# Optimization experiments

Hardware: AMD Instinct MI355X
Metric: run time of the kernel (lower is better)

Reference implementation:

```python
import jax, jax.numpy as jnp
import numpy as np

N_NODES = 100000
N_EDGES = 1600000
D_FEAT = 64


def setup_inputs() -> dict:
    key = jax.random.key(0)
    k1, k2, k3, k4 = jax.random.split(key, 4)
    row = jnp.sort(jax.random.randint(k1, (N_EDGES,), 0, N_NODES, dtype=jnp.int32))
    col = jax.random.randint(k2, (N_EDGES,), 0, N_NODES, dtype=jnp.int32)
    values = jax.random.uniform(k3, (N_EDGES,), dtype=jnp.float32)
    x = jax.random.normal(k4, (N_NODES, D_FEAT), dtype=jnp.float32)
    return {"row": row, "col": col, "values": values, "x": x}


def reference(row, col, values, x):
    # spmm_scatter: out[row[e]] += values[e] * x[col[e]]  (gather-multiply-scatter)
    msgs = x[col] * values[:, None]                      # [E, d]
    out = jax.ops.segment_sum(msgs, row, num_segments=x.shape[0])  # [N, d]
    return out
```

## Files before the change

kernel.cpp:

```cpp
#include <hip/hip_runtime.h>
#include <hip/hip_fp16.h>


constexpr int D  = 64;
constexpr int DV = 16;
constexpr int DH = 16;

struct __align__(8) h4 { __half2 a, b; };

__global__ __launch_bounds__(256) void prep_kernel(
    const int* __restrict__ row,
    const float4* __restrict__ x4,
    h4* __restrict__ xh,
    int* __restrict__ row_ptr,
    int nEdges, int n4, int nNodes)
{
    const int i = blockIdx.x * blockDim.x + threadIdx.x;
    if (i < n4) {
        const float4 v = x4[i];
        h4 h;
        h.a = __float22half2_rn(make_float2(v.x, v.y));
        h.b = __float22half2_rn(make_float2(v.z, v.w));
        xh[i] = h;
    }
    if (i < nEdges) {
        const int r    = row[i];
        const int prev = (i == 0) ? -1 : row[i - 1];
        for (int n = prev + 1; n <= r; ++n) row_ptr[n] = i;
        if (i == nEdges - 1)
            for (int n = r + 1; n <= nNodes; ++n) row_ptr[n] = nEdges;
    }
}

__global__ __launch_bounds__(256) void spmm_h(
    const int* __restrict__ row_ptr,
    const int* __restrict__ col,
    const float* __restrict__ val,
    const h4* __restrict__ xh,
    float4* __restrict__ out4,
    int nNodes)
{
    const int wid = (blockIdx.x * blockDim.x + threadIdx.x) >> 6;
    if (wid >= nNodes) return;
    const int lane  = threadIdx.x & 63;
    const int group = lane >> 4;
    const int sub   = lane & 15;

    const int start = row_ptr[wid];
    const int end   = row_ptr[wid + 1];

    float4 acc = {0.f, 0.f, 0.f, 0.f};
    for (int e = start + group; e < end; e += 16) {
        const int e1 = e + 4, e2 = e + 8, e3 = e + 12;
        const int   c0 = col[e];
        const float v0 = val[e];
        int c1 = c0, c2 = c0, c3 = c0;
        float v1 = 0.f, v2 = 0.f, v3 = 0.f;
        if (e1 < end) { c1 = col[e1]; v1 = val[e1]; }
        if (e2 < end) { c2 = col[e2]; v2 = val[e2]; }
        if (e3 < end) { c3 = col[e3]; v3 = val[e3]; }
        const h4 p0 = xh[(size_t)c0 * DH + sub];
        const h4 p1 = xh[(size_t)c1 * DH + sub];
        const h4 p2 = xh[(size_t)c2 * DH + sub];
        const h4 p3 = xh[(size_t)c3 * DH + sub];
        float2 f;
        f = __half22float2(p0.a); acc.x = fmaf(v0, f.x, acc.x); acc.y = fmaf(v0, f.y, acc.y);
        f = __half22float2(p0.b); acc.z = fmaf(v0, f.x, acc.z); acc.w = fmaf(v0, f.y, acc.w);
        f = __half22float2(p1.a); acc.x = fmaf(v1, f.x, acc.x); acc.y = fmaf(v1, f.y, acc.y);
        f = __half22float2(p1.b); acc.z = fmaf(v1, f.x, acc.z); acc.w = fmaf(v1, f.y, acc.w);
        f = __half22float2(p2.a); acc.x = fmaf(v2, f.x, acc.x); acc.y = fmaf(v2, f.y, acc.y);
        f = __half22float2(p2.b); acc.z = fmaf(v2, f.x, acc.z); acc.w = fmaf(v2, f.y, acc.w);
        f = __half22float2(p3.a); acc.x = fmaf(v3, f.x, acc.x); acc.y = fmaf(v3, f.y, acc.y);
        f = __half22float2(p3.b); acc.z = fmaf(v3, f.x, acc.z); acc.w = fmaf(v3, f.y, acc.w);
    }

    #pragma unroll
    for (int off = 16; off <= 32; off <<= 1) {
        acc.x += __shfl_xor(acc.x, off, 64);
        acc.y += __shfl_xor(acc.y, off, 64);
        acc.z += __shfl_xor(acc.z, off, 64);
        acc.w += __shfl_xor(acc.w, off, 64);
    }
    if (group == 0) out4[(size_t)wid * DV + sub] = acc;
}

__global__ __launch_bounds__(256) void spmm_psearch(
    const int* __restrict__ row,
    const int* __restrict__ col,
    const float* __restrict__ val,
    const float4* __restrict__ x4,
    float4* __restrict__ out4,
    int nEdges, int nNodes)
{
    const int wid = (blockIdx.x * blockDim.x + threadIdx.x) >> 6;
    if (wid >= nNodes) return;
    const int lane  = threadIdx.x & 63;
    const int group = lane >> 4;
    const int sub   = lane & 15;

    int lo = 0, hi = nEdges;
    const int t0 = wid;
    while (hi > lo) {
        const int span = hi - lo + 1;
        if (span <= 64) {
            const int idx = lo + lane;
            const bool lt = (idx <= hi) && (idx < nEdges) && (row[idx] < t0);
            lo += __popcll(__ballot(lt));
            break;
        }
        const int step = (span + 63) >> 6;
        const int idx  = lo + lane * step;
        const bool lt  = (idx <= hi) && (idx < nEdges) && (row[idx] < t0);
        const int  c   = __popcll(__ballot(lt));
        if (c == 0) { hi = lo; break; }
        const int new_lo = lo + (c - 1) * step + 1;
        if (c < 64) hi = lo + c * step;
        lo = new_lo;
    }
    const int start = lo;
    const int t1 = wid + 1;
    int end = start;
    for (;;) {
        const int idx = end + lane;
        const bool lt = (idx < nEdges) && (row[idx] < t1);
        const int  c  = __popcll(__ballot(lt));
        end += c;
        if (c < 64) break;
    }

    float4 acc = {0.f, 0.f, 0.f, 0.f};
    for (int e = start + group; e < end; e += 8) {
        const int e1 = e + 4;
        const int   c0 = col[e];
        const float v0 = val[e];
        int c1 = c0; float v1 = 0.f;
        if (e1 < end) { c1 = col[e1]; v1 = val[e1]; }
        const float4 x0 = x4[(size_t)c0 * DV + sub];
        const float4 x1 = x4[(size_t)c1 * DV + sub];
        acc.x = fmaf(v0, x0.x, acc.x); acc.y = fmaf(v0, x0.y, acc.y);
        acc.z = fmaf(v0, x0.z, acc.z); acc.w = fmaf(v0, x0.w, acc.w);
        acc.x = fmaf(v1, x1.x, acc.x); acc.y = fmaf(v1, x1.y, acc.y);
        acc.z = fmaf(v1, x1.z, acc.z); acc.w = fmaf(v1, x1.w, acc.w);
    }
    #pragma unroll
    for (int off = 16; off <= 32; off <<= 1) {
        acc.x += __shfl_xor(acc.x, off, 64);
        acc.y += __shfl_xor(acc.y, off, 64);
        acc.z += __shfl_xor(acc.z, off, 64);
        acc.w += __shfl_xor(acc.w, off, 64);
    }
    if (group == 0) out4[(size_t)wid * DV + sub] = acc;
}

extern "C" void kernel_launch(void* const* d_in, const int* in_sizes, int n_in,
                              void* d_out, int out_size, void* d_ws, size_t ws_size,
                              hipStream_t stream)
{
    const int*    row  = (const int*)   d_in[0];
    const int*    col  = (const int*)   d_in[1];
    const float*  val  = (const float*) d_in[2];
    const float4* x4   = (const float4*)d_in[3];
    float4*       out4 = (float4*)d_out;

    const int nEdges = in_sizes[0];
    const int nNodes = out_size / D;
    const int n4     = nNodes * DV;

    const dim3 block(256);
    const dim3 gridMain(((size_t)nNodes * 64 + 255) / 256);

    const size_t rp_bytes = (size_t)(nNodes + 1) * sizeof(int);
    const size_t xh_off   = (rp_bytes + 255) & ~(size_t)255;
    const size_t need     = xh_off + (size_t)nNodes * D * sizeof(__half);

    if (ws_size >= need) {
        int* row_ptr = (int*)d_ws;
        h4*  xh      = (h4*)((char*)d_ws + xh_off);
        const int prep_n = (nEdges > n4) ? nEdges : n4;
        prep_kernel<<<dim3((prep_n + 255) / 256), block, 0, stream>>>(
            row, x4, xh, row_ptr, nEdges, n4, nNodes);
        spmm_h<<<gridMain, block, 0, stream>>>(
            row_ptr, (const int*)d_in[1], val, xh, out4, nNodes);
    } else {
        spmm_psearch<<<gridMain, block, 0, stream>>>(
            row, (const int*)d_in[1], val, x4, out4, nEdges, nNodes);
    }
}
```

Before: 135.4 us.

## Use 16-byte half8 gathers and cooperative edge-index loads with shuffle broadcast

Widens each lane's fp16 gather of x from 8 to 16 bytes, so 8 lanes cover a 64-feature row and 8 edge groups run in parallel. The first 64 edges of a row have their col/val loaded once per wave, one per lane, and are then broadcast with shuffles, replacing redundant per-group index loads. The prep kernel now converts two float4s per thread. The cost is more shuffles, a three-step reduction over 8 accumulators, and a tail loop for rows with more than 64 edges.

```diff
diff --git a/kernel.cpp b/kernel.cpp
--- a/kernel.cpp
+++ b/kernel.cpp
@@ -2,25 +2,28 @@
 #include <hip/hip_fp16.h>
 
 
-constexpr int D  = 64;
-constexpr int DV = 16;
-constexpr int DH = 16;
-
-struct __align__(8) h4 { __half2 a, b; };
+constexpr int D   = 64;
+constexpr int DV  = 16;
+constexpr int DH8 = 8;
+
+struct __align__(16) h8 { __half2 a, b, c, d; };
 
 __global__ __launch_bounds__(256) void prep_kernel(
     const int* __restrict__ row,
     const float4* __restrict__ x4,
-    h4* __restrict__ xh,
+    h8* __restrict__ xh,
     int* __restrict__ row_ptr,
-    int nEdges, int n4, int nNodes)
+    int nEdges, int n8, int nNodes)
 {
     const int i = blockIdx.x * blockDim.x + threadIdx.x;
-    if (i < n4) {
-        const float4 v = x4[i];
-        h4 h;
-        h.a = __float22half2_rn(make_float2(v.x, v.y));
-        h.b = __float22half2_rn(make_float2(v.z, v.w));
+    if (i < n8) {
+        const float4 lo = x4[2 * i];
+        const float4 hi = x4[2 * i + 1];
+        h8 h;
+        h.a = __float22half2_rn(make_float2(lo.x, lo.y));
+        h.b = __float22half2_rn(make_float2(lo.z, lo.w));
+        h.c = __float22half2_rn(make_float2(hi.x, hi.y));
+        h.d = __float22half2_rn(make_float2(hi.z, hi.w));
         xh[i] = h;
     }
     if (i < nEdges) {
@@ -32,56 +35,77 @@
     }
 }
 
-__global__ __launch_bounds__(256) void spmm_h(
+__device__ __forceinline__ void fma_h8(const h8& p, float v, float4& a0, float4& a1)
+{
+    float2 f;
+    f = __half22float2(p.a); a0.x = fmaf(v, f.x, a0.x); a0.y = fmaf(v, f.y, a0.y);
+    f = __half22float2(p.b); a0.z = fmaf(v, f.x, a0.z); a0.w = fmaf(v, f.y, a0.w);
+    f = __half22float2(p.c); a1.x = fmaf(v, f.x, a1.x); a1.y = fmaf(v, f.y, a1.y);
+    f = __half22float2(p.d); a1.z = fmaf(v, f.x, a1.z); a1.w = fmaf(v, f.y, a1.w);
+}
+
+__global__ __launch_bounds__(256) void spmm_h8(
     const int* __restrict__ row_ptr,
     const int* __restrict__ col,
     const float* __restrict__ val,
-    const h4* __restrict__ xh,
+    const h8* __restrict__ xh,
     float4* __restrict__ out4,
     int nNodes)
 {
     const int wid = (blockIdx.x * blockDim.x + threadIdx.x) >> 6;
     if (wid >= nNodes) return;
-    const int lane  = threadIdx.x & 63;
-    const int group = lane >> 4;
-    const int sub   = lane & 15;
-
-    const int start = row_ptr[wid];
-    const int end   = row_ptr[wid + 1];
-
-    float4 acc = {0.f, 0.f, 0.f, 0.f};
-    for (int e = start + group; e < end; e += 16) {
-        const int e1 = e + 4, e2 = e + 8, e3 = e + 12;
-        const int   c0 = col[e];
-        const float v0 = val[e];
-        int c1 = c0, c2 = c0, c3 = c0;
-        float v1 = 0.f, v2 = 0.f, v3 = 0.f;
+    const int lane = threadIdx.x & 63;
+    const int g    = lane >> 3;
+    const int sub  = lane & 7;
+
+    const int uw    = __builtin_amdgcn_readfirstlane(wid);
+    const int start = row_ptr[uw];
+    const int end   = row_ptr[uw + 1];
+    const int deg   = end - start;
+
+    const int  eL  = start + lane;
+    const bool okL = eL < end;
+    const int   cv = okL ? col[eL] : 0;
+    const float vv = okL ? val[eL] : 0.f;
+
+    float4 a0 = {0.f, 0.f, 0.f, 0.f};
+    float4 a1 = {0.f, 0.f, 0.f, 0.f};
+
+    const int it64 = min((deg + 15) >> 4, 4);
+    for (int it = 0; it < it64; ++it) {
+        const int s0 = it * 16 + 2 * g;
+        const int   c0 = __shfl(cv, s0, 64);
+        const float v0 = __shfl(vv, s0, 64);
+        const int   c1 = __shfl(cv, s0 + 1, 64);
+        const float v1 = __shfl(vv, s0 + 1, 64);
+        const h8 p0 = xh[(size_t)c0 * DH8 + sub];
+        const h8 p1 = xh[(size_t)c1 * DH8 + sub];
+        fma_h8(p0, v0, a0, a1);
+        fma_h8(p1, v1, a0, a1);
+    }
+
+    for (int ebase = start + 64; ebase < end; ebase += 16) {
+        const int e0 = ebase + 2 * g, e1 = e0 + 1;
+        int c0 = 0, c1 = 0; float v0 = 0.f, v1 = 0.f;
+        if (e0 < end) { c0 = col[e0]; v0 = val[e0]; }
         if (e1 < end) { c1 = col[e1]; v1 = val[e1]; }
-        if (e2 < end) { c2 = col[e2]; v2 = val[e2]; }
-        if (e3 < end) { c3 = col[e3]; v3 = val[e3]; }
-        const h4 p0 = xh[(size_t)c0 * DH + sub];
-        const h4 p1 = xh[(size_t)c1 * DH + sub];
-        const h4 p2 = xh[(size_t)c2 * DH + sub];
-        const h4 p3 = xh[(size_t)c3 * DH + sub];
-        float2 f;
-        f = __half22float2(p0.a); acc.x = fmaf(v0, f.x, acc.x); acc.y = fmaf(v0, f.y, acc.y);
-        f = __half22float2(p0.b); acc.z = fmaf(v0, f.x, acc.z); acc.w = fmaf(v0, f.y, acc.w);
-        f = __half22float2(p1.a); acc.x = fmaf(v1, f.x, acc.x); acc.y = fmaf(v1, f.y, acc.y);
-        f = __half22float2(p1.b); acc.z = fmaf(v1, f.x, acc.z); acc.w = fmaf(v1, f.y, acc.w);
-        f = __half22float2(p2.a); acc.x = fmaf(v2, f.x, acc.x); acc.y = fmaf(v2, f.y, acc.y);
-        f = __half22float2(p2.b); acc.z = fmaf(v2, f.x, acc.z); acc.w = fmaf(v2, f.y, acc.w);
-        f = __half22float2(p3.a); acc.x = fmaf(v3, f.x, acc.x); acc.y = fmaf(v3, f.y, acc.y);
-        f = __half22float2(p3.b); acc.z = fmaf(v3, f.x, acc.z); acc.w = fmaf(v3, f.y, acc.w);
+        const h8 p0 = xh[(size_t)c0 * DH8 + sub];
+        const h8 p1 = xh[(size_t)c1 * DH8 + sub];
+        fma_h8(p0, v0, a0, a1);
+        fma_h8(p1, v1, a0, a1);
     }
 
     #pragma unroll
-    for (int off = 16; off <= 32; off <<= 1) {
-        acc.x += __shfl_xor(acc.x, off, 64);
-        acc.y += __shfl_xor(acc.y, off, 64);
-        acc.z += __shfl_xor(acc.z, off, 64);
-        acc.w += __shfl_xor(acc.w, off, 64);
-    }
-    if (group == 0) out4[(size_t)wid * DV + sub] = acc;
+    for (int off = 8; off <= 32; off <<= 1) {
+        a0.x += __shfl_xor(a0.x, off, 64); a0.y += __shfl_xor(a0.y, off, 64);
+        a0.z += __shfl_xor(a0.z, off, 64); a0.w += __shfl_xor(a0.w, off, 64);
+        a1.x += __shfl_xor(a1.x, off, 64); a1.y += __shfl_xor(a1.y, off, 64);
+        a1.z += __shfl_xor(a1.z, off, 64); a1.w += __shfl_xor(a1.w, off, 64);
+    }
+    if (g == 0) {
+        out4[(size_t)wid * DV + 2 * sub]     = a0;
+        out4[(size_t)wid * DV + 2 * sub + 1] = a1;
+    }
 }
 
 __global__ __launch_bounds__(256) void spmm_psearch(
@@ -164,7 +188,7 @@
 
     const int nEdges = in_sizes[0];
     const int nNodes = out_size / D;
-    const int n4     = nNodes * DV;
+    const int n8     = nNodes * DH8;
 
     const dim3 block(256);
     const dim3 gridMain(((size_t)nNodes * 64 + 255) / 256);
@@ -175,14 +199,14 @@
 
     if (ws_size >= need) {
         int* row_ptr = (int*)d_ws;
-        h4*  xh      = (h4*)((char*)d_ws + xh_off);
-        const int prep_n = (nEdges > n4) ? nEdges : n4;
+        h8*  xh      = (h8*)((char*)d_ws + xh_off);
+        const int prep_n = (nEdges > n8) ? nEdges : n8;
         prep_kernel<<<dim3((prep_n + 255) / 256), block, 0, stream>>>(
-            row, x4, xh, row_ptr, nEdges, n4, nNodes);
-        spmm_h<<<gridMain, block, 0, stream>>>(
-            row_ptr, (const int*)d_in[1], val, xh, out4, nNodes);
+            row, x4, xh, row_ptr, nEdges, n8, nNodes);
+        spmm_h8<<<gridMain, block, 0, stream>>>(
+            row_ptr, col, val, xh, out4, nNodes);
     } else {
         spmm_psearch<<<gridMain, block, 0, stream>>>(
-            row, (const int*)d_in[1], val, x4, out4, nEdges, nNodes);
-    }
-}
+            row, col, val, x4, out4, nEdges, nNodes);
+    }
+}
```

New measurement: 124.5 us. -8.0%, faster.
